# Performance work log

Measured on AMD Instinct MI355X. Metric: run time of the kernel, lower is better.

The kernel has to match this reference:

```python
import jax, jax.numpy as jnp
import numpy as np

N_NODES = 50000
N_EDGES = 800000
C_IN = 128
C_OUT = 128


def setup_inputs() -> dict:
    key = jax.random.key(0)
    k1, k2, k3, k4 = jax.random.split(key, 4)
    x = jax.random.normal(k1, (N_NODES, C_IN), dtype=jnp.float32)
    edge_index = jax.random.randint(k2, (2, N_EDGES), 0, N_NODES, dtype=jnp.int64)
    # Linear(in, out): weight [out, in], bias [out]
    W = jax.random.normal(k3, (C_OUT, C_IN), dtype=jnp.float32) * (1.0 / np.sqrt(C_IN))
    b = jax.random.normal(k4, (C_OUT,), dtype=jnp.float32) * 0.01
    return {"x": x, "edge_index": edge_index, "W": W, "b": b}


def reference(x, edge_index, W, b):
    # GCN layer: out = D^{-1/2} (A + I) D^{-1/2} x W^T + b
    # Implemented as sparse gather/segment-sum (same math as the dense
    # adjacency matmul in the original, without the O(N^2) blowup).
    n = x.shape[0]
    loops = jnp.arange(n, dtype=edge_index.dtype)
    row = jnp.concatenate([edge_index[0], loops])  # [E+N]
    col = jnp.concatenate([edge_index[1], loops])  # [E+N]
    # degree over col index (as in pyg_utils.degree(edge_index[1], ...))
    ones = jnp.ones(row.shape[0], dtype=x.dtype)
    deg = jax.ops.segment_sum(ones, col, num_segments=n)
    deg_inv_sqrt = jnp.where(deg > 0, jax.lax.rsqrt(deg), 0.0).astype(x.dtype)
    norm = deg_inv_sqrt[row] * deg_inv_sqrt[col]  # [E+N]
    # aggregate: out[i] = sum_{(i,j) in edges} norm * x[j]
    msgs = x[col] * norm[:, None]  # [E+N, C_in]
    agg = jax.ops.segment_sum(msgs, row, num_segments=n)  # [N, C_in]
    return agg @ W.T + b
```

## Files before the change

kernel.cpp:

```cpp
#include <hip/hip_runtime.h>
#include <hip/hip_bf16.h>
#include <hip/hip_fp16.h>

#define C 128
#define NCH 32768
#define CN 2
#define CNODES (CN * NCH)
#define BE 64

typedef _Float16 f16x8 __attribute__((ext_vector_type(8)));
typedef _Float16 f16x4 __attribute__((ext_vector_type(4)));
typedef float f32x4 __attribute__((ext_vector_type(4)));

__global__ __launch_bounds__(256) void k_hist(
        const int* __restrict__ row, const int* __restrict__ col,
        unsigned char* __restrict__ part_row, unsigned char* __restrict__ part_col,
        unsigned char* __restrict__ tag, int E) {
    __shared__ unsigned lh[NCH / 4];
    int bid = blockIdx.x;
    int side = (bid >= CN * BE) ? 1 : 0;
    int lb = side ? bid - CN * BE : bid;
    int c = lb >> 6;
    int b = lb & (BE - 1);
    int tid = threadIdx.x;
    for (int i = tid * 4; i < NCH / 4; i += 1024) {
        lh[i] = 0u; lh[i + 1] = 0u; lh[i + 2] = 0u; lh[i + 3] = 0u;
    }
    __syncthreads();
    int EPB = (E + BE - 1) / BE;
    int base = b * EPB;
    int end = min(base + EPB, E);
    const int* src = side ? col : row;

#define PROC_ROW(rv, ev)                                                  \
    if (((unsigned)(rv) >> 15) == (unsigned)c) {                          \
        int loc = (rv) & (NCH - 1);                                       \
        unsigned sh = ((unsigned)loc & 3u) << 3;                          \
        unsigned old = atomicAdd(&lh[loc >> 2], 1u << sh);                \
        tag[ev] = (unsigned char)((old >> sh) & 0xffu);                   \
    }
#define PROC_COL(rv)                                                      \
    if (((unsigned)(rv) >> 15) == (unsigned)c) {                          \
        int loc = (rv) & (NCH - 1);                                       \
        atomicAdd(&lh[loc >> 2], 1u << (((unsigned)loc & 3u) << 3));      \
    }
    int nv = 0;
    if ((((uintptr_t)(src + base)) & 15) == 0) nv = (end - base) >> 2;
    const int4* src4 = (const int4*)(src + base);
    if (!side) {
        for (int it = tid; it < nv; it += 256) {
            int4 v = src4[it];
            int e0 = base + it * 4;
            PROC_ROW(v.x, e0);
            PROC_ROW(v.y, e0 + 1);
            PROC_ROW(v.z, e0 + 2);
            PROC_ROW(v.w, e0 + 3);
        }
        for (int e = base + nv * 4 + tid; e < end; e += 256) {
            int r = src[e];
            PROC_ROW(r, e);
        }
    } else {
        for (int it = tid; it < nv; it += 256) {
            int4 v = src4[it];
            PROC_COL(v.x);
            PROC_COL(v.y);
            PROC_COL(v.z);
            PROC_COL(v.w);
        }
        for (int e = base + nv * 4 + tid; e < end; e += 256) {
            int r = src[e];
            PROC_COL(r);
        }
    }
#undef PROC_ROW
#undef PROC_COL
    __syncthreads();
    unsigned* dst = (unsigned*)((side ? part_col : part_row) + (size_t)b * CNODES + c * NCH);
    for (int i = tid; i < NCH / 4; i += 256) dst[i] = lh[i];
}

__global__ __launch_bounds__(256) void k_reduce_scan(
        unsigned char* __restrict__ part_row, const unsigned char* __restrict__ part_col,
        unsigned* __restrict__ start, unsigned* __restrict__ bsum,
        float* __restrict__ dis, int n) {
    __shared__ unsigned s[256];
    int t = threadIdx.x;
    int i = blockIdx.x * 256 + t;
    unsigned acc = 0;
    if (i < n) {
#pragma unroll 8
        for (int b = 0; b < BE; ++b) {
            size_t off = (size_t)b * CNODES + i;
            unsigned v = part_row[off];
            part_row[off] = (unsigned char)acc;
            acc += v;
        }
        unsigned d = 0;
#pragma unroll 8
        for (int b = 0; b < BE; ++b) d += part_col[(size_t)b * CNODES + i];
        dis[i] = rsqrtf((float)(d + 1u));
    }
    unsigned v = acc;
    s[t] = v;
    __syncthreads();
    for (int off = 1; off < 256; off <<= 1) {
        unsigned add = (t >= off) ? s[t - off] : 0u;
        __syncthreads();
        s[t] += add;
        __syncthreads();
    }
    if (i < n) start[i] = s[t] - v;
    if (t == 255) bsum[blockIdx.x] = s[t];
}

__global__ __launch_bounds__(256) void k_scan_final(unsigned* __restrict__ start,
                                                    const unsigned* __restrict__ bsum,
                                                    int n, int E) {
    __shared__ unsigned s[256];
    int t = threadIdx.x;
    int bid = blockIdx.x;
    s[t] = (t < bid) ? bsum[t] : 0u;
    __syncthreads();
    for (int off = 128; off > 0; off >>= 1) {
        if (t < off) s[t] += s[t + off];
        __syncthreads();
    }
    unsigned base = s[0];
    int i = bid * 256 + t;
    if (i < n) start[i] += base;
    if (i == n) start[i] = (unsigned)E;
}

__global__ __launch_bounds__(256) void k_scatter_gemm(
        const int* __restrict__ row, const int* __restrict__ col,
        const unsigned char* __restrict__ tag, const unsigned char* __restrict__ boff,
        const unsigned* __restrict__ start, int* __restrict__ scol, int E, int SB,
        const float* __restrict__ A, const float* __restrict__ W,
        const float* __restrict__ dis, __half* __restrict__ Z16, int n) {
    __shared__ char lds[128 * 256];
    int bid = blockIdx.x;
    int tid = threadIdx.x;
    if (bid < SB) {
        int e = bid * 256 + tid;
        if (e < E) {
            int EPB = (E + BE - 1) / BE;
            unsigned b = (unsigned)e / (unsigned)EPB;
            int r = row[e];
            unsigned p = start[r] + boff[(size_t)b * CNODES + r] + tag[e];
            scol[p] = col[e];
        }
        return;
    }
    int w = tid >> 6, lane = tid & 63;
    int m0 = (bid - SB) * 128;

#pragma unroll
    for (int i = 0; i < 16; ++i) {
        int fidx = i * 256 + tid;
        int nr = fidx >> 5;
        int c4 = fidx & 31;
        float4 wv = *(const float4*)(W + (size_t)nr * C + c4 * 4);
        f16x4 hh = {(_Float16)wv.x, (_Float16)wv.y, (_Float16)wv.z, (_Float16)wv.w};
        unsigned byte = (unsigned)(nr * 256 + c4 * 8);
        byte ^= (unsigned)((nr & 7) << 4);
        *(f16x4*)(lds + byte) = hh;
    }
    __syncthreads();

    int rbase = m0 + w * 32;
    int q = lane >> 4, rl = lane & 15;
    float dm[2];
#pragma unroll
    for (int mt = 0; mt < 2; ++mt) {
        int r = rbase + mt * 16 + rl;
        dm[mt] = (r < n) ? dis[r] : 0.f;
    }
    f32x4 acc[2][8] = {};
#pragma unroll
    for (int kc = 0; kc < 4; ++kc) {
        f16x8 af[2];
#pragma unroll
        for (int mt = 0; mt < 2; ++mt) {
            int r = rbase + mt * 16 + rl;
            float4 x0 = make_float4(0.f, 0.f, 0.f, 0.f), x1 = x0;
            if (r < n) {
                const float* srcx = A + (size_t)r * C + kc * 32 + q * 8;
                x0 = *(const float4*)srcx;
                x1 = *(const float4*)(srcx + 4);
            }
            float s = dm[mt];
            af[mt][0] = (_Float16)(x0.x * s);
            af[mt][1] = (_Float16)(x0.y * s);
            af[mt][2] = (_Float16)(x0.z * s);
            af[mt][3] = (_Float16)(x0.w * s);
            af[mt][4] = (_Float16)(x1.x * s);
            af[mt][5] = (_Float16)(x1.y * s);
            af[mt][6] = (_Float16)(x1.z * s);
            af[mt][7] = (_Float16)(x1.w * s);
        }
#pragma unroll
        for (int nt = 0; nt < 8; ++nt) {
            int nrow = nt * 16 + rl;
            unsigned byte = (unsigned)(nrow * 256 + kc * 64 + q * 16);
            byte ^= (unsigned)((nrow & 7) << 4);
            f16x8 bf = *(f16x8*)(lds + byte);
            acc[0][nt] = __builtin_amdgcn_mfma_f32_16x16x32_f16(af[0], bf, acc[0][nt], 0, 0, 0);
            acc[1][nt] = __builtin_amdgcn_mfma_f32_16x16x32_f16(af[1], bf, acc[1][nt], 0, 0, 0);
        }
    }
    __syncthreads();

#pragma unroll
    for (int mt = 0; mt < 2; ++mt)
#pragma unroll
        for (int nt = 0; nt < 8; ++nt)
#pragma unroll
            for (int i = 0; i < 4; ++i) {
                int row_l = w * 32 + mt * 16 + q * 4 + i;
                int colh = nt * 16 + rl;
                unsigned byte = (unsigned)(row_l * 256 + colh * 2);
                byte ^= (unsigned)((row_l & 7) << 4);
                *(_Float16*)(lds + byte) = (_Float16)acc[mt][nt][i];
            }
    __syncthreads();

#pragma unroll
    for (int it = 0; it < 8; ++it) {
        int idx = it * 256 + tid;
        int row_l = idx >> 4, c8 = idx & 15;
        unsigned byte = (unsigned)(row_l * 256 + c8 * 16);
        byte ^= (unsigned)((row_l & 7) << 4);
        uint4 v = *(uint4*)(lds + byte);
        int gr = m0 + row_l;
        if (gr < n) *(uint4*)(Z16 + (size_t)gr * C + c8 * 8) = v;
    }
}

__global__ __launch_bounds__(256) void k_agg(const __half2* __restrict__ Z2,
                                             const int* __restrict__ scol,
                                             const unsigned* __restrict__ start,
                                             const float* __restrict__ dis,
                                             const float* __restrict__ bias,
                                             float* __restrict__ out, int n) {
    int wid = threadIdx.x >> 6;
    int lane = threadIdx.x & 63;
    int r = blockIdx.x * 4 + wid;
    if (r >= n) return;
    unsigned s0 = start[r], s1 = start[r + 1];
    float dr = dis[r];
    float2 acc = __half22float2(Z2[(size_t)r * 64 + lane]);
    unsigned k = s0;
    for (; k + 16 <= s1; k += 16) {
        int c[16];
#pragma unroll
        for (int j = 0; j < 16; ++j) c[j] = scol[k + j];
        __half2 h[16];
#pragma unroll
        for (int j = 0; j < 16; ++j) h[j] = Z2[(size_t)c[j] * 64 + lane];
        float2 p0 = {0.f, 0.f}, p1 = {0.f, 0.f};
#pragma unroll
        for (int j = 0; j < 16; j += 2) {
            float2 f0 = __half22float2(h[j]);
            float2 f1 = __half22float2(h[j + 1]);
            p0.x += f0.x; p0.y += f0.y;
            p1.x += f1.x; p1.y += f1.y;
        }
        acc.x += p0.x + p1.x;
        acc.y += p0.y + p1.y;
    }
    for (; k + 4 <= s1; k += 4) {
        int c[4];
#pragma unroll
        for (int j = 0; j < 4; ++j) c[j] = scol[k + j];
        __half2 h[4];
#pragma unroll
        for (int j = 0; j < 4; ++j) h[j] = Z2[(size_t)c[j] * 64 + lane];
#pragma unroll
        for (int j = 0; j < 4; ++j) {
            float2 f = __half22float2(h[j]);
            acc.x += f.x;
            acc.y += f.y;
        }
    }
    for (; k < s1; ++k) {
        float2 f = __half22float2(Z2[(size_t)scol[k] * 64 + lane]);
        acc.x += f.x;
        acc.y += f.y;
    }
    float2 bv = *(const float2*)(bias + lane * 2);
    float2 o;
    o.x = bv.x + dr * acc.x;
    o.y = bv.y + dr * acc.y;
    *(float2*)(out + (size_t)r * C + lane * 2) = o;
}

extern "C" void kernel_launch(void* const* d_in, const int* in_sizes, int n_in,
                              void* d_out, int out_size, void* d_ws, size_t ws_size,
                              hipStream_t stream) {
    const float* x  = (const float*)d_in[0];
    const int*   ei = (const int*)d_in[1];
    const float* W  = (const float*)d_in[2];
    const float* b  = (const float*)d_in[3];
    float* out = (float*)d_out;

    int n = in_sizes[0] / C;
    int E = in_sizes[1] / 2;
    const int* row = ei;
    const int* col = ei + E;

    char* p = (char*)d_ws;
    size_t sz_part = (((size_t)BE * CNODES) + 511) & ~(size_t)511;
    size_t sz_n    = (((size_t)n * 4) + 511) & ~(size_t)511;
    size_t sz_n1   = (((size_t)(n + 1) * 4) + 511) & ~(size_t)511;
    size_t sz_E1   = (((size_t)E) + 511) & ~(size_t)511;
    size_t sz_E4   = (((size_t)E * 4) + 511) & ~(size_t)511;
    size_t off = 0;
    unsigned char*  part_row = (unsigned char*)(p + off);  off += sz_part;
    unsigned char*  part_col = (unsigned char*)(p + off);  off += sz_part;
    unsigned*       start    = (unsigned*)(p + off);       off += sz_n1;
    float*          dis      = (float*)(p + off);          off += sz_n;
    unsigned*       bsum     = (unsigned*)(p + off);       off += 4096;
    unsigned char*  tag      = (unsigned char*)(p + off);  off += sz_E1;
    int*            scol     = (int*)(p + off);            off += sz_E4;
    __half*         z16      = (__half*)(p + off);

    int NT = 256;
    int NB = (n + NT - 1) / NT;
    int SB = (E + NT - 1) / NT;
    int GB = (n + 127) / 128;

    k_hist<<<2 * CN * BE, NT, 0, stream>>>(row, col, part_row, part_col, tag, E);
    k_reduce_scan<<<NB, NT, 0, stream>>>(part_row, part_col, start, bsum, dis, n);
    k_scan_final<<<NB, NT, 0, stream>>>(start, bsum, n, E);
    k_scatter_gemm<<<SB + GB, NT, 0, stream>>>(row, col, tag, part_row, start, scol,
                                               E, SB, x, W, dis, z16, n);
    k_agg<<<(n + 3) / 4, NT, 0, stream>>>((const __half2*)z16, scol, start, dis, b, out, n);
}
```

Before: 88.64 us.

## Split Z into channel passes and raise histogram block count for aggregation

The fp16 Z matrix is now stored as four 32-channel slabs, and the aggregation kernel runs one pass per slab. Each wavefront processes four edges at once (16 lanes per edge) and reduces them with shuffles, so each pass's gathered slab is smaller and more cache friendly. The histogram partitioning doubles its block count (BE 128), and the per-block edge count is rounded to a multiple of four so the int4 loads are always aligned. In exchange, the scol/start lists are read four times, the histogram partial buffers double in size, and shuffle reductions are added.

```diff
diff --git a/kernel.cpp b/kernel.cpp
--- a/kernel.cpp
+++ b/kernel.cpp
@@ -6,7 +6,8 @@
 #define NCH 32768
 #define CN 2
 #define CNODES (CN * NCH)
-#define BE 64
+#define BE 128
+#define NPASS 4
 
 typedef _Float16 f16x8 __attribute__((ext_vector_type(8)));
 typedef _Float16 f16x4 __attribute__((ext_vector_type(4)));
@@ -15,19 +16,18 @@
 __global__ __launch_bounds__(256) void k_hist(
         const int* __restrict__ row, const int* __restrict__ col,
         unsigned char* __restrict__ part_row, unsigned char* __restrict__ part_col,
-        unsigned char* __restrict__ tag, int E) {
+        unsigned char* __restrict__ tag, int E, int EPB) {
     __shared__ unsigned lh[NCH / 4];
     int bid = blockIdx.x;
     int side = (bid >= CN * BE) ? 1 : 0;
     int lb = side ? bid - CN * BE : bid;
-    int c = lb >> 6;
+    int c = lb >> 7;
     int b = lb & (BE - 1);
     int tid = threadIdx.x;
     for (int i = tid * 4; i < NCH / 4; i += 1024) {
         lh[i] = 0u; lh[i + 1] = 0u; lh[i + 2] = 0u; lh[i + 3] = 0u;
     }
     __syncthreads();
-    int EPB = (E + BE - 1) / BE;
     int base = b * EPB;
     int end = min(base + EPB, E);
     const int* src = side ? col : row;
@@ -44,8 +44,7 @@
         int loc = (rv) & (NCH - 1);                                       \
         atomicAdd(&lh[loc >> 2], 1u << (((unsigned)loc & 3u) << 3));      \
     }
-    int nv = 0;
-    if ((((uintptr_t)(src + base)) & 15) == 0) nv = (end - base) >> 2;
+    int nv = (end > base) ? ((end - base) >> 2) : 0;
     const int4* src4 = (const int4*)(src + base);
     if (!side) {
         for (int it = tid; it < nv; it += 256) {
@@ -135,7 +134,8 @@
 __global__ __launch_bounds__(256) void k_scatter_gemm(
         const int* __restrict__ row, const int* __restrict__ col,
         const unsigned char* __restrict__ tag, const unsigned char* __restrict__ boff,
-        const unsigned* __restrict__ start, int* __restrict__ scol, int E, int SB,
+        const unsigned* __restrict__ start, int* __restrict__ scol,
+        int E, int EPB, int SB,
         const float* __restrict__ A, const float* __restrict__ W,
         const float* __restrict__ dis, __half* __restrict__ Z16, int n) {
     __shared__ char lds[128 * 256];
@@ -144,7 +144,6 @@
     if (bid < SB) {
         int e = bid * 256 + tid;
         if (e < E) {
-            int EPB = (E + BE - 1) / BE;
             unsigned b = (unsigned)e / (unsigned)EPB;
             int r = row[e];
             unsigned p = start[r] + boff[(size_t)b * CNODES + r] + tag[e];
@@ -233,66 +232,67 @@
         byte ^= (unsigned)((row_l & 7) << 4);
         uint4 v = *(uint4*)(lds + byte);
         int gr = m0 + row_l;
-        if (gr < n) *(uint4*)(Z16 + (size_t)gr * C + c8 * 8) = v;
-    }
-}
-
-__global__ __launch_bounds__(256) void k_agg(const __half2* __restrict__ Z2,
+        if (gr < n) {
+            int pass = c8 >> 2;
+            int sub = c8 & 3;
+            *(uint4*)(Z16 + ((size_t)pass * n + gr) * 32 + sub * 8) = v;
+        }
+    }
+}
+
+__global__ __launch_bounds__(256) void k_agg(const __half2* __restrict__ Zc,
                                              const int* __restrict__ scol,
                                              const unsigned* __restrict__ start,
                                              const float* __restrict__ dis,
                                              const float* __restrict__ bias,
-                                             float* __restrict__ out, int n) {
+                                             float* __restrict__ out, int n, int RPB) {
+    int bid = blockIdx.x;
+    int pass = bid / RPB;
+    int rb = bid - pass * RPB;
     int wid = threadIdx.x >> 6;
     int lane = threadIdx.x & 63;
-    int r = blockIdx.x * 4 + wid;
-    if (r >= n) return;
-    unsigned s0 = start[r], s1 = start[r + 1];
-    float dr = dis[r];
-    float2 acc = __half22float2(Z2[(size_t)r * 64 + lane]);
-    unsigned k = s0;
-    for (; k + 16 <= s1; k += 16) {
-        int c[16];
-#pragma unroll
-        for (int j = 0; j < 16; ++j) c[j] = scol[k + j];
-        __half2 h[16];
-#pragma unroll
-        for (int j = 0; j < 16; ++j) h[j] = Z2[(size_t)c[j] * 64 + lane];
-        float2 p0 = {0.f, 0.f}, p1 = {0.f, 0.f};
-#pragma unroll
-        for (int j = 0; j < 16; j += 2) {
-            float2 f0 = __half22float2(h[j]);
-            float2 f1 = __half22float2(h[j + 1]);
-            p0.x += f0.x; p0.y += f0.y;
-            p1.x += f1.x; p1.y += f1.y;
-        }
-        acc.x += p0.x + p1.x;
-        acc.y += p0.y + p1.y;
-    }
-    for (; k + 4 <= s1; k += 4) {
-        int c[4];
-#pragma unroll
-        for (int j = 0; j < 4; ++j) c[j] = scol[k + j];
-        __half2 h[4];
-#pragma unroll
-        for (int j = 0; j < 4; ++j) h[j] = Z2[(size_t)c[j] * 64 + lane];
-#pragma unroll
-        for (int j = 0; j < 4; ++j) {
-            float2 f = __half22float2(h[j]);
-            acc.x += f.x;
-            acc.y += f.y;
-        }
-    }
-    for (; k < s1; ++k) {
-        float2 f = __half22float2(Z2[(size_t)scol[k] * 64 + lane]);
-        acc.x += f.x;
-        acc.y += f.y;
-    }
-    float2 bv = *(const float2*)(bias + lane * 2);
-    float2 o;
-    o.x = bv.x + dr * acc.x;
-    o.y = bv.y + dr * acc.y;
-    *(float2*)(out + (size_t)r * C + lane * 2) = o;
+    int slot = lane >> 4;
+    int cp = lane & 15;
+    const __half2* Z = Zc + (size_t)pass * n * 16;
+    int r0 = rb * 8 + wid * 2;
+
+#pragma unroll
+    for (int rr = 0; rr < 2; ++rr) {
+        int r = r0 + rr;
+        if (r >= n) continue;
+        unsigned s0 = start[r], s1 = start[r + 1];
+        float dr = dis[r];
+        float2 acc = {0.f, 0.f};
+        if (slot == 0) acc = __half22float2(Z[(size_t)r * 16 + cp]);
+        unsigned k = s0;
+        for (; k + 8 <= s1; k += 8) {
+            unsigned ka = k + slot, kb = k + 4 + slot;
+            int ca = scol[ka], cb = scol[kb];
+            __half2 ha = Z[(size_t)ca * 16 + cp];
+            __half2 hb = Z[(size_t)cb * 16 + cp];
+            float2 fa = __half22float2(ha), fb = __half22float2(hb);
+            acc.x += fa.x + fb.x;
+            acc.y += fa.y + fb.y;
+        }
+        for (; k < s1; k += 4) {
+            unsigned ke = k + slot;
+            if (ke < s1) {
+                int c = scol[ke];
+                float2 f = __half22float2(Z[(size_t)c * 16 + cp]);
+                acc.x += f.x;
+                acc.y += f.y;
+            }
+        }
+        acc.x += __shfl_xor(acc.x, 16); acc.y += __shfl_xor(acc.y, 16);
+        acc.x += __shfl_xor(acc.x, 32); acc.y += __shfl_xor(acc.y, 32);
+        if (slot == 0) {
+            float2 bv = *(const float2*)(bias + pass * 32 + cp * 2);
+            float2 o;
+            o.x = bv.x + dr * acc.x;
+            o.y = bv.y + dr * acc.y;
+            *(float2*)(out + (size_t)r * C + pass * 32 + cp * 2) = o;
+        }
+    }
 }
 
 extern "C" void kernel_launch(void* const* d_in, const int* in_sizes, int n_in,
@@ -327,13 +327,16 @@
 
     int NT = 256;
     int NB = (n + NT - 1) / NT;
+    int EPB = (((E + BE - 1) / BE) + 3) & ~3;
     int SB = (E + NT - 1) / NT;
     int GB = (n + 127) / 128;
-
-    k_hist<<<2 * CN * BE, NT, 0, stream>>>(row, col, part_row, part_col, tag, E);
+    int RPB = (n + 7) / 8;
+
+    k_hist<<<2 * CN * BE, NT, 0, stream>>>(row, col, part_row, part_col, tag, E, EPB);
     k_reduce_scan<<<NB, NT, 0, stream>>>(part_row, part_col, start, bsum, dis, n);
     k_scan_final<<<NB, NT, 0, stream>>>(start, bsum, n, E);
     k_scatter_gemm<<<SB + GB, NT, 0, stream>>>(row, col, tag, part_row, start, scol,
-                                               E, SB, x, W, dis, z16, n);
-    k_agg<<<(n + 3) / 4, NT, 0, stream>>>((const __half2*)z16, scol, start, dis, b, out, n);
-}
+                                               E, EPB, SB, x, W, dis, z16, n);
+    k_agg<<<NPASS * RPB, NT, 0, stream>>>((const __half2*)z16, scol, start, dis, b,
+                                          out, n, RPB);
+}
```

Measured after the change: 131.0 us. 47.8% more time.

## Split each wavefront into four edge slots with 16-byte row gathers

Applied to the files above, without the earlier changes.

The aggregation kernel now splits each 64-lane wavefront into four 16-lane slots. Each slot gathers a different neighbor row with 16-byte loads, instead of all lanes reading 4 bytes from the same row. Partial sums are combined with cross-slot shuffles, and one slot writes the output with float4 stores. This raises the number of independent memory requests in flight per wave and cuts the load instruction count. In exchange it adds shuffle reductions, and only a quarter of the lanes are active for the final store.

```diff
diff --git a/kernel.cpp b/kernel.cpp
--- a/kernel.cpp
+++ b/kernel.cpp
@@ -237,7 +237,16 @@
     }
 }
 
-__global__ __launch_bounds__(256) void k_agg(const __half2* __restrict__ Z2,
+__device__ __forceinline__ void add8(uint4 v, float2& a0, float2& a1,
+                                     float2& a2, float2& a3) {
+    float2 f;
+    f = __half22float2(*(__half2*)&v.x); a0.x += f.x; a0.y += f.y;
+    f = __half22float2(*(__half2*)&v.y); a1.x += f.x; a1.y += f.y;
+    f = __half22float2(*(__half2*)&v.z); a2.x += f.x; a2.y += f.y;
+    f = __half22float2(*(__half2*)&v.w); a3.x += f.x; a3.y += f.y;
+}
+
+__global__ __launch_bounds__(256) void k_agg(const __half* __restrict__ Z16,
                                              const int* __restrict__ scol,
                                              const unsigned* __restrict__ start,
                                              const float* __restrict__ dis,
@@ -245,54 +254,61 @@
                                              float* __restrict__ out, int n) {
     int wid = threadIdx.x >> 6;
     int lane = threadIdx.x & 63;
+    int slot = lane >> 4;
+    int g = lane & 15;
     int r = blockIdx.x * 4 + wid;
     if (r >= n) return;
     unsigned s0 = start[r], s1 = start[r + 1];
     float dr = dis[r];
-    float2 acc = __half22float2(Z2[(size_t)r * 64 + lane]);
+    const uint4* Z4 = (const uint4*)Z16;
+    float2 a0 = {0.f, 0.f}, a1 = a0, a2 = a0, a3 = a0;
+    if (slot == 0) {
+        uint4 v = Z4[(size_t)r * 16 + g];
+        add8(v, a0, a1, a2, a3);
+    }
     unsigned k = s0;
     for (; k + 16 <= s1; k += 16) {
-        int c[16];
-#pragma unroll
-        for (int j = 0; j < 16; ++j) c[j] = scol[k + j];
-        __half2 h[16];
-#pragma unroll
-        for (int j = 0; j < 16; ++j) h[j] = Z2[(size_t)c[j] * 64 + lane];
-        float2 p0 = {0.f, 0.f}, p1 = {0.f, 0.f};
-#pragma unroll
-        for (int j = 0; j < 16; j += 2) {
-            float2 f0 = __half22float2(h[j]);
-            float2 f1 = __half22float2(h[j + 1]);
-            p0.x += f0.x; p0.y += f0.y;
-            p1.x += f1.x; p1.y += f1.y;
-        }
-        acc.x += p0.x + p1.x;
-        acc.y += p0.y + p1.y;
-    }
-    for (; k + 4 <= s1; k += 4) {
-        int c[4];
-#pragma unroll
-        for (int j = 0; j < 4; ++j) c[j] = scol[k + j];
-        __half2 h[4];
-#pragma unroll
-        for (int j = 0; j < 4; ++j) h[j] = Z2[(size_t)c[j] * 64 + lane];
-#pragma unroll
-        for (int j = 0; j < 4; ++j) {
-            float2 f = __half22float2(h[j]);
-            acc.x += f.x;
-            acc.y += f.y;
-        }
-    }
-    for (; k < s1; ++k) {
-        float2 f = __half22float2(Z2[(size_t)scol[k] * 64 + lane]);
-        acc.x += f.x;
-        acc.y += f.y;
-    }
-    float2 bv = *(const float2*)(bias + lane * 2);
-    float2 o;
-    o.x = bv.x + dr * acc.x;
-    o.y = bv.y + dr * acc.y;
-    *(float2*)(out + (size_t)r * C + lane * 2) = o;
+        int c0 = scol[k + slot];
+        int c1 = scol[k + 4 + slot];
+        int c2 = scol[k + 8 + slot];
+        int c3 = scol[k + 12 + slot];
+        uint4 v0 = Z4[(size_t)c0 * 16 + g];
+        uint4 v1 = Z4[(size_t)c1 * 16 + g];
+        uint4 v2 = Z4[(size_t)c2 * 16 + g];
+        uint4 v3 = Z4[(size_t)c3 * 16 + g];
+        add8(v0, a0, a1, a2, a3);
+        add8(v1, a0, a1, a2, a3);
+        add8(v2, a0, a1, a2, a3);
+        add8(v3, a0, a1, a2, a3);
+    }
+    for (; k < s1; k += 4) {
+        unsigned ke = k + slot;
+        if (ke < s1) {
+            int c = scol[ke];
+            uint4 v = Z4[(size_t)c * 16 + g];
+            add8(v, a0, a1, a2, a3);
+        }
+    }
+    a0.x += __shfl_xor(a0.x, 16); a0.y += __shfl_xor(a0.y, 16);
+    a1.x += __shfl_xor(a1.x, 16); a1.y += __shfl_xor(a1.y, 16);
+    a2.x += __shfl_xor(a2.x, 16); a2.y += __shfl_xor(a2.y, 16);
+    a3.x += __shfl_xor(a3.x, 16); a3.y += __shfl_xor(a3.y, 16);
+    a0.x += __shfl_xor(a0.x, 32); a0.y += __shfl_xor(a0.y, 32);
+    a1.x += __shfl_xor(a1.x, 32); a1.y += __shfl_xor(a1.y, 32);
+    a2.x += __shfl_xor(a2.x, 32); a2.y += __shfl_xor(a2.y, 32);
+    a3.x += __shfl_xor(a3.x, 32); a3.y += __shfl_xor(a3.y, 32);
+    if (slot == 0) {
+        float4 b0 = *(const float4*)(bias + g * 8);
+        float4 b1 = *(const float4*)(bias + g * 8 + 4);
+        float4 o0, o1;
+        o0.x = b0.x + dr * a0.x; o0.y = b0.y + dr * a0.y;
+        o0.z = b0.z + dr * a1.x; o0.w = b0.w + dr * a1.y;
+        o1.x = b1.x + dr * a2.x; o1.y = b1.y + dr * a2.y;
+        o1.z = b1.z + dr * a3.x; o1.w = b1.w + dr * a3.y;
+        float* op = out + (size_t)r * C + g * 8;
+        *(float4*)op = o0;
+        *(float4*)(op + 4) = o1;
+    }
 }
 
 extern "C" void kernel_launch(void* const* d_in, const int* in_sizes, int n_in,
@@ -335,5 +351,5 @@
     k_scan_final<<<NB, NT, 0, stream>>>(start, bsum, n, E);
     k_scatter_gemm<<<SB + GB, NT, 0, stream>>>(row, col, tag, part_row, start, scol,
                                                E, SB, x, W, dis, z16, n);
-    k_agg<<<(n + 3) / 4, NT, 0, stream>>>((const __half2*)z16, scol, start, dis, b, out, n);
-}
+    k_agg<<<(n + 3) / 4, NT, 0, stream>>>(z16, scol, start, dis, b, out, n);
+}
```

Result: faster. 81.23 us (-8.4%).
